# Optimization experiments

Hardware: AMD Instinct MI355X
Metric: run time of the kernel (lower is better)

The kernel has to match this reference:

```python
import jax, jax.numpy as jnp
import numpy as np


def setup_inputs() -> dict:
    key = jax.random.key(0)
    k1, k2, k3 = jax.random.split(key, 3)
    B, N = 128, 900
    x = jax.random.normal(k1, (B, N), dtype=jnp.float32)
    # true heart-rate frequencies in a realistic band (Hz)
    f_true = jax.random.uniform(k2, (B,), dtype=jnp.float32, minval=1.0, maxval=2.5)
    fs = 30.0 + jax.random.uniform(k3, (B,), dtype=jnp.float32, minval=-0.5, maxval=0.5)
    return {
        "x": x,
        "f_true": f_true,
        "fs": fs,
        "delta": 0.1,
        "sampling_f": 0.01,
        "f_min": 0.66,
        "f_max": 3.0,
    }


def _psd(freqs, x, fs, n):
    # freqs: [B, F], x: [B, N], fs: [B], n: [N]
    # Goertzel-style single-bin DFT power: (sum x*cos)^2 + (sum x*sin)^2
    ang = (2.0 * np.pi) * freqs[:, :, None] * n[None, None, :] / fs[:, None, None]  # [B,F,N]
    c = jnp.einsum('bfn,bn->bf', jnp.cos(ang), x)
    s = jnp.einsum('bfn,bn->bf', jnp.sin(ang), x)
    return c * c + s * s


def reference(x, f_true, fs, delta, sampling_f, f_min, f_max):
    B, N = x.shape
    n = jnp.arange(N, dtype=x.dtype)
    s = sampling_f

    # wanted bins: arange(f_true - delta, f_true + delta + s, s) -> static offsets around f_true
    off_w = jnp.asarray(np.arange(-delta, delta + s, s), dtype=x.dtype)  # [Fw] (~21)
    f_w = f_true[:, None] + off_w[None, :]                                # [B, Fw]

    # unwanted bins: two grids with data-dependent extents -> static max length + mask
    k_max = int(np.ceil((f_max - f_min) / s)) + 2
    k = jnp.arange(k_max, dtype=x.dtype)                                  # [K]
    f_u1 = jnp.broadcast_to(f_min + k * s, (B, k_max))                    # grid from f_min
    m1 = f_u1 < (f_true[:, None] - delta)                                 # arange end exclusive
    f_u2 = f_true[:, None] + delta + s + k[None, :] * s                   # grid from f_true+delta+s
    m2 = f_u2 < (f_max + s)

    p_w = _psd(f_w, x, fs, n)                                             # [B, Fw]
    p_u1 = _psd(f_u1, x, fs, n)                                           # [B, K]
    p_u2 = _psd(f_u2, x, fs, n)                                           # [B, K]

    term1 = p_w.mean(axis=1)
    cnt = m1.sum(axis=1) + m2.sum(axis=1)
    term2 = ((p_u1 * m1).sum(axis=1) + (p_u2 * m2).sum(axis=1)) / cnt.astype(x.dtype)
    snr = 10.0 * jnp.log10(term1 / term2)                                 # [B]
    return -snr.mean()
```

## Files before the change

### kernel.cpp

```cpp
#include <hip/hip_runtime.h>
#include <math.h>


#define WAVES 8
#define BPW   4
#define BINS_PER_BLOCK (WAVES * BPW)

template<int NG>
__global__ __launch_bounds__(64 * WAVES)
void psd_radix4(const float* __restrict__ x,
                const float* __restrict__ f_true,
                const float* __restrict__ fs,
                double* __restrict__ partW,
                double* __restrict__ partU,
                int* __restrict__ cntbuf,
                int N, int Fw, int K, int bpb, int ng_rt,
                double wstart, double wstep,
                float f_min_f, float s_f, float delta_f, float fmax_s_f)
{
    const int ng   = (NG > 0) ? NG : ng_rt;
    const int npad = ng << 8;
    extern __shared__ float xs[];
    __shared__ int    s_mc1[WAVES], s_mc2[WAVES];
    __shared__ double s_dw[WAVES], s_du[WAVES], s_inv;

    const int b    = blockIdx.x / bpb;
    const int tile = blockIdx.x - b * bpb;
    const int tid  = threadIdx.x;
    const int lane = tid & 63;
    const int w    = tid >> 6;

    for (int i = tid; i < npad; i += blockDim.x)
        xs[i] = (i < N) ? x[(size_t)b * N + i] : 0.0f;

    const float ft   = f_true[b];
    const float thr1 = __fsub_rn(ft, delta_f);

    int mc1 = 0, mc2 = 0;
    for (int i = tid; i < 2 * K; i += blockDim.x) {
        if (i < K) {
            float fu = __fadd_rn(f_min_f, __fmul_rn((float)i, s_f));
            mc1 += (fu < thr1);
        } else {
            int j = i - K;
            float fu = __fadd_rn(__fadd_rn(__fadd_rn(ft, delta_f), s_f),
                                 __fmul_rn((float)j, s_f));
            mc2 += (fu < fmax_s_f);
        }
    }
    #pragma unroll
    for (int off = 32; off; off >>= 1) {
        mc1 += __shfl_xor(mc1, off);
        mc2 += __shfl_xor(mc2, off);
    }
    if (lane == 0) { s_mc1[w] = mc1; s_mc2[w] = mc2; }
    if (tid == 0)  s_inv = 1.0 / (double)fs[b];
    __syncthreads();

    int m1 = 0, m2 = 0;
    #pragma unroll
    for (int i = 0; i < WAVES; ++i) { m1 += s_mc1[i]; m2 += s_mc2[i]; }
    const int nb = Fw + m1 + m2;
    const double inv = s_inv;

    const int u0 = (tile * WAVES + w) * BPW;

    float P[BPW], Q[BPW];
    #pragma unroll
    for (int p = 0; p < BPW; ++p) { P[p] = 0.0f; Q[p] = 0.0f; }

    if (u0 < nb) {
        float c1[BPW], s1[BPW], c2[BPW], s2[BPW], c3[BPW], s3[BPW];
        float cR[BPW], sR[BPW], Cg[BPW], Sg[BPW];
        #pragma unroll
        for (int p = 0; p < BPW; ++p) {
            const int u = u0 + p;
            float f;
            if (u < Fw)
                f = __fadd_rn(ft, (float)(wstart + (double)u * wstep));
            else if (u < Fw + m1)
                f = __fadd_rn(f_min_f, __fmul_rn((float)(u - Fw), s_f));
            else
                f = __fadd_rn(__fadd_rn(__fadd_rn(ft, delta_f), s_f),
                              __fmul_rn((float)(u - Fw - m1), s_f));
            const double r = (double)f * inv;
            double t0 = r * (double)lane; t0 -= rint(t0);
            double ts = r * 64.0;         ts -= rint(ts);
            c1[p] = __builtin_amdgcn_cosf((float)ts);
            s1[p] = __builtin_amdgcn_sinf((float)ts);
            Cg[p] = __builtin_amdgcn_cosf((float)t0);
            Sg[p] = __builtin_amdgcn_sinf((float)t0);
            c2[p] = fmaf(c1[p], c1[p], -(s1[p] * s1[p]));
            s2[p] = c1[p] * s1[p]; s2[p] += s2[p];
            c3[p] = fmaf(c2[p], c1[p], -(s2[p] * s1[p]));
            s3[p] = fmaf(s2[p], c1[p],  (c2[p] * s1[p]));
            cR[p] = fmaf(c2[p], c2[p], -(s2[p] * s2[p]));
            sR[p] = c2[p] * s2[p]; sR[p] += sR[p];
        }

        for (int g = 0; g < ng; ++g) {
            const int base = (g << 8) + lane;
            float xv0 = xs[base];
            float xv1 = xs[base + 64];
            float xv2 = xs[base + 128];
            float xv3 = xs[base + 192];
            #pragma unroll
            for (int p = 0; p < BPW; ++p) {
                float pr = fmaf(xv1, c1[p], xv0);
                pr = fmaf(xv2, c2[p], pr);
                pr = fmaf(xv3, c3[p], pr);
                float pi = xv1 * s1[p];
                pi = fmaf(xv2, s2[p], pi);
                pi = fmaf(xv3, s3[p], pi);
                P[p] = fmaf(pr, Cg[p], P[p]);
                P[p] = fmaf(-pi, Sg[p], P[p]);
                Q[p] = fmaf(pr, Sg[p], Q[p]);
                Q[p] = fmaf(pi, Cg[p], Q[p]);
                if (g != ng - 1) {
                    float cn = fmaf(Cg[p], cR[p], -(Sg[p] * sR[p]));
                    float sn = fmaf(Sg[p], cR[p],  (Cg[p] * sR[p]));
                    Cg[p] = cn; Sg[p] = sn;
                }
            }
        }
    }

    double dw = 0.0, du = 0.0;
    #pragma unroll
    for (int p = 0; p < BPW; ++p) {
        float a = P[p], q = Q[p];
        #pragma unroll
        for (int off = 32; off; off >>= 1) {
            a += __shfl_xor(a, off);
            q += __shfl_xor(q, off);
        }
        if (lane == 0) {
            const int u = u0 + p;
            if (u < nb) {
                float pw = fmaf(a, a, q * q);
                if (u < Fw) dw += (double)pw; else du += (double)pw;
            }
        }
    }
    if (lane == 0) { s_dw[w] = dw; s_du[w] = du; }
    __syncthreads();

    if (tid == 0) {
        double SW = 0.0, SU = 0.0;
        #pragma unroll
        for (int i = 0; i < WAVES; ++i) { SW += s_dw[i]; SU += s_du[i]; }
        partW[(size_t)b * bpb + tile] = SW;
        partU[(size_t)b * bpb + tile] = SU;
        if (tile == 0) cntbuf[b] = m1 + m2;
    }
}

__global__ __launch_bounds__(128)
void finish_kernel(const double* __restrict__ partW,
                   const double* __restrict__ partU,
                   const int* __restrict__ cntbuf,
                   float* __restrict__ out,
                   int Fw, int bpb, int B)
{
    const int tid  = threadIdx.x;
    const int lane = tid & 63;
    const int w    = tid >> 6;
    __shared__ double s_v[2];

    double v = 0.0;
    for (int b = tid; b < B; b += blockDim.x) {
        double SW = 0.0, SU = 0.0;
        for (int t = 0; t < bpb; ++t) {
            SW += partW[(size_t)b * bpb + t];
            SU += partU[(size_t)b * bpb + t];
        }
        v += 10.0 * log10((SW / (double)Fw) / (SU / (double)cntbuf[b]));
    }
    #pragma unroll
    for (int off = 32; off; off >>= 1) v += __shfl_xor(v, off);
    if (lane == 0) s_v[w] = v;
    __syncthreads();
    if (tid == 0) out[0] = (float)(-((s_v[0] + s_v[1]) / (double)B));
}

extern "C" void kernel_launch(void* const* d_in, const int* in_sizes, int n_in,
                              void* d_out, int out_size, void* d_ws, size_t ws_size,
                              hipStream_t stream) {
    const float* x      = (const float*)d_in[0];
    const float* f_true = (const float*)d_in[1];
    const float* fs     = (const float*)d_in[2];
    const double delta = 0.1, s = 0.01, f_min = 0.66, f_max = 3.0;

    const int B = in_sizes[1];
    const int N = in_sizes[0] / B;

    const double wstart = -delta;
    const double wstop  = delta + s;
    const double wstep  = s;
    const int Fw = (int)ceil((wstop - wstart) / wstep);
    const int K  = (int)ceil((f_max - f_min) / s) + 2;

    const int maxu  = Fw + (int)((f_max - f_min - 2.0 * delta) / s) + 8;
    const int bpb   = (maxu + BINS_PER_BLOCK - 1) / BINS_PER_BLOCK;
    const int niter = (N + 63) / 64;
    const int ng    = (niter + 3) / 4;

    const float f_min_f  = (float)f_min;
    const float s_f      = (float)s;
    const float delta_f  = (float)delta;
    const float fmax_s_f = (float)(f_max + s);

    char* base = (char*)d_ws;
    double* partW  = (double*)base;
    double* partU  = partW + (size_t)B * bpb;
    int*    cntbuf = (int*)(partU + (size_t)B * bpb);

    const size_t shmem = (size_t)ng * 256 * sizeof(float);
    dim3 grid(B * bpb), block(64 * WAVES);

    if (ng == 4)
        psd_radix4<4><<<grid, block, shmem, stream>>>(
            x, f_true, fs, partW, partU, cntbuf, N, Fw, K, bpb, ng,
            wstart, wstep, f_min_f, s_f, delta_f, fmax_s_f);
    else
        psd_radix4<0><<<grid, block, shmem, stream>>>(
            x, f_true, fs, partW, partU, cntbuf, N, Fw, K, bpb, ng,
            wstart, wstep, f_min_f, s_f, delta_f, fmax_s_f);

    finish_kernel<<<1, 128, 0, stream>>>(
        partW, partU, cntbuf, (float*)d_out, Fw, bpb, B);
}
```

Measured before the change: 18.13 us.

## Double waves per block, vectorize loads, ballot counts, and packed shuffle reductions

The block grows from 8 to 16 waves, which halves the number of blocks per batch row. The x tile is loaded into shared memory as float4, and the mask counts use ballot/popcount instead of shuffle reductions. The eight separate wave reductions of P and Q become a packed butterfly that sums several bins at once. Partials are stored as double2 and the finish kernel is templated on the tile count so its loop unrolls. The packed reduction uses fixed lane-to-bin indexing that assumes BPW==4, and the larger blocks may reduce how many blocks are resident at once.

Result: slower. 26.84 us (+48.0%).

```diff
diff --git a/kernel.cpp b/kernel.cpp
--- a/kernel.cpp
+++ b/kernel.cpp
@@ -2,17 +2,16 @@
 #include <math.h>
 
 
-#define WAVES 8
+#define WAVES 16
 #define BPW   4
 #define BINS_PER_BLOCK (WAVES * BPW)
 
 template<int NG>
-__global__ __launch_bounds__(64 * WAVES)
+__global__ __launch_bounds__(64 * WAVES, 8)
 void psd_radix4(const float* __restrict__ x,
                 const float* __restrict__ f_true,
                 const float* __restrict__ fs,
-                double* __restrict__ partW,
-                double* __restrict__ partU,
+                double2* __restrict__ part2,
                 int* __restrict__ cntbuf,
                 int N, int Fw, int K, int bpb, int ng_rt,
                 double wstart, double wstep,
@@ -21,7 +20,7 @@
     const int ng   = (NG > 0) ? NG : ng_rt;
     const int npad = ng << 8;
     extern __shared__ float xs[];
-    __shared__ int    s_mc1[WAVES], s_mc2[WAVES];
+    __shared__ int    s_c1[WAVES], s_c2[WAVES];
     __shared__ double s_dw[WAVES], s_du[WAVES], s_inv;
 
     const int b    = blockIdx.x / bpb;
@@ -30,36 +29,45 @@
     const int lane = tid & 63;
     const int w    = tid >> 6;
 
-    for (int i = tid; i < npad; i += blockDim.x)
-        xs[i] = (i < N) ? x[(size_t)b * N + i] : 0.0f;
+    {
+        const int nf4 = N >> 2;
+        float4* xs4 = reinterpret_cast<float4*>(xs);
+        const float4* xr = reinterpret_cast<const float4*>(x + (size_t)b * N);
+        for (int i = tid; i < (npad >> 2); i += blockDim.x)
+            xs4[i] = (i < nf4) ? xr[i] : make_float4(0.f, 0.f, 0.f, 0.f);
+        if (N & 3)
+            for (int i = (N & ~3) + tid; i < N; i += blockDim.x)
+                xs[i] = x[(size_t)b * N + i];
+    }
 
     const float ft   = f_true[b];
     const float thr1 = __fsub_rn(ft, delta_f);
 
-    int mc1 = 0, mc2 = 0;
-    for (int i = tid; i < 2 * K; i += blockDim.x) {
-        if (i < K) {
-            float fu = __fadd_rn(f_min_f, __fmul_rn((float)i, s_f));
-            mc1 += (fu < thr1);
-        } else {
-            int j = i - K;
-            float fu = __fadd_rn(__fadd_rn(__fadd_rn(ft, delta_f), s_f),
-                                 __fmul_rn((float)j, s_f));
-            mc2 += (fu < fmax_s_f);
-        }
-    }
-    #pragma unroll
-    for (int off = 32; off; off >>= 1) {
-        mc1 += __shfl_xor(mc1, off);
-        mc2 += __shfl_xor(mc2, off);
-    }
-    if (lane == 0) { s_mc1[w] = mc1; s_mc2[w] = mc2; }
-    if (tid == 0)  s_inv = 1.0 / (double)fs[b];
+    {
+        int c1 = 0, c2 = 0;
+        for (int i = tid; i < ((2 * K + (int)blockDim.x - 1) / (int)blockDim.x) * (int)blockDim.x;
+             i += blockDim.x) {
+            bool p1 = false, p2 = false;
+            if (i < K) {
+                float fu = __fadd_rn(f_min_f, __fmul_rn((float)i, s_f));
+                p1 = fu < thr1;
+            } else if (i < 2 * K) {
+                int j = i - K;
+                float fu = __fadd_rn(__fadd_rn(__fadd_rn(ft, delta_f), s_f),
+                                     __fmul_rn((float)j, s_f));
+                p2 = fu < fmax_s_f;
+            }
+            c1 += __popcll(__ballot(p1));
+            c2 += __popcll(__ballot(p2));
+        }
+        if (lane == 0) { s_c1[w] = c1; s_c2[w] = c2; }
+    }
+    if (tid == 0) s_inv = 1.0 / (double)fs[b];
     __syncthreads();
 
     int m1 = 0, m2 = 0;
     #pragma unroll
-    for (int i = 0; i < WAVES; ++i) { m1 += s_mc1[i]; m2 += s_mc2[i]; }
+    for (int i = 0; i < WAVES; ++i) { m1 += s_c1[i]; m2 += s_c2[i]; }
     const int nb = Fw + m1 + m2;
     const double inv = s_inv;
 
@@ -70,7 +78,7 @@
     for (int p = 0; p < BPW; ++p) { P[p] = 0.0f; Q[p] = 0.0f; }
 
     if (u0 < nb) {
-        float c1[BPW], s1[BPW], c2[BPW], s2[BPW], c3[BPW], s3[BPW];
+        float c1c[BPW], s1c[BPW], c2c[BPW], s2c[BPW], c3c[BPW], s3c[BPW];
         float cR[BPW], sR[BPW], Cg[BPW], Sg[BPW];
         #pragma unroll
         for (int p = 0; p < BPW; ++p) {
@@ -86,16 +94,16 @@
             const double r = (double)f * inv;
             double t0 = r * (double)lane; t0 -= rint(t0);
             double ts = r * 64.0;         ts -= rint(ts);
-            c1[p] = __builtin_amdgcn_cosf((float)ts);
-            s1[p] = __builtin_amdgcn_sinf((float)ts);
-            Cg[p] = __builtin_amdgcn_cosf((float)t0);
-            Sg[p] = __builtin_amdgcn_sinf((float)t0);
-            c2[p] = fmaf(c1[p], c1[p], -(s1[p] * s1[p]));
-            s2[p] = c1[p] * s1[p]; s2[p] += s2[p];
-            c3[p] = fmaf(c2[p], c1[p], -(s2[p] * s1[p]));
-            s3[p] = fmaf(s2[p], c1[p],  (c2[p] * s1[p]));
-            cR[p] = fmaf(c2[p], c2[p], -(s2[p] * s2[p]));
-            sR[p] = c2[p] * s2[p]; sR[p] += sR[p];
+            c1c[p] = __builtin_amdgcn_cosf((float)ts);
+            s1c[p] = __builtin_amdgcn_sinf((float)ts);
+            Cg[p]  = __builtin_amdgcn_cosf((float)t0);
+            Sg[p]  = __builtin_amdgcn_sinf((float)t0);
+            c2c[p] = fmaf(c1c[p], c1c[p], -(s1c[p] * s1c[p]));
+            s2c[p] = c1c[p] * s1c[p]; s2c[p] += s2c[p];
+            c3c[p] = fmaf(c2c[p], c1c[p], -(s2c[p] * s1c[p]));
+            s3c[p] = fmaf(s2c[p], c1c[p],  (c2c[p] * s1c[p]));
+            cR[p]  = fmaf(c2c[p], c2c[p], -(s2c[p] * s2c[p]));
+            sR[p]  = c2c[p] * s2c[p]; sR[p] += sR[p];
         }
 
         for (int g = 0; g < ng; ++g) {
@@ -106,12 +114,12 @@
             float xv3 = xs[base + 192];
             #pragma unroll
             for (int p = 0; p < BPW; ++p) {
-                float pr = fmaf(xv1, c1[p], xv0);
-                pr = fmaf(xv2, c2[p], pr);
-                pr = fmaf(xv3, c3[p], pr);
-                float pi = xv1 * s1[p];
-                pi = fmaf(xv2, s2[p], pi);
-                pi = fmaf(xv3, s3[p], pi);
+                float pr = fmaf(xv1, c1c[p], xv0);
+                pr = fmaf(xv2, c2c[p], pr);
+                pr = fmaf(xv3, c3c[p], pr);
+                float pi = xv1 * s1c[p];
+                pi = fmaf(xv2, s2c[p], pi);
+                pi = fmaf(xv3, s3c[p], pi);
                 P[p] = fmaf(pr, Cg[p], P[p]);
                 P[p] = fmaf(-pi, Sg[p], P[p]);
                 Q[p] = fmaf(pr, Sg[p], Q[p]);
@@ -125,62 +133,85 @@
         }
     }
 
-    double dw = 0.0, du = 0.0;
-    #pragma unroll
-    for (int p = 0; p < BPW; ++p) {
-        float a = P[p], q = Q[p];
-        #pragma unroll
-        for (int off = 32; off; off >>= 1) {
-            a += __shfl_xor(a, off);
-            q += __shfl_xor(q, off);
-        }
-        if (lane == 0) {
-            const int u = u0 + p;
-            if (u < nb) {
-                float pw = fmaf(a, a, q * q);
-                if (u < Fw) dw += (double)pw; else du += (double)pw;
-            }
-        }
-    }
-    if (lane == 0) { s_dw[w] = dw; s_du[w] = du; }
+    {
+        const bool selA = (lane & 32) != 0;
+        const bool selB = (lane & 16) != 0;
+        const bool selC = (lane & 8)  != 0;
+        float F0, F1, F2, F3, G0, G1, H;
+        { float t1 = P[0] + __shfl_xor(P[0], 32);
+          float t2 = Q[0] + __shfl_xor(Q[0], 32); F0 = selA ? t2 : t1; }
+        { float t1 = P[1] + __shfl_xor(P[1], 32);
+          float t2 = Q[1] + __shfl_xor(Q[1], 32); F1 = selA ? t2 : t1; }
+        { float t1 = P[2] + __shfl_xor(P[2], 32);
+          float t2 = Q[2] + __shfl_xor(Q[2], 32); F2 = selA ? t2 : t1; }
+        { float t1 = P[3] + __shfl_xor(P[3], 32);
+          float t2 = Q[3] + __shfl_xor(Q[3], 32); F3 = selA ? t2 : t1; }
+        { float t1 = F0 + __shfl_xor(F0, 16);
+          float t2 = F1 + __shfl_xor(F1, 16); G0 = selB ? t2 : t1; }
+        { float t1 = F2 + __shfl_xor(F2, 16);
+          float t2 = F3 + __shfl_xor(F3, 16); G1 = selB ? t2 : t1; }
+        { float t1 = G0 + __shfl_xor(G0, 8);
+          float t2 = G1 + __shfl_xor(G1, 8); H = selC ? t2 : t1; }
+        H += __shfl_xor(H, 4);
+        H += __shfl_xor(H, 2);
+        H += __shfl_xor(H, 1);
+
+        float qv = __shfl_xor(H, 32);
+        float pw = fmaf(H, H, qv * qv);
+        const int p = (((lane >> 3) & 1) << 1) | ((lane >> 4) & 1);
+        const int u = u0 + p;
+        const bool rep = ((lane & 7) == 0) && !selA;
+        float cw = (rep && u < Fw) ? pw : 0.0f;
+        float cu = (rep && u >= Fw && u < nb) ? pw : 0.0f;
+        cw += __shfl_xor(cw, 8);  cw += __shfl_xor(cw, 16);
+        cu += __shfl_xor(cu, 8);  cu += __shfl_xor(cu, 16);
+        if (lane == 0) { s_dw[w] = (double)cw; s_du[w] = (double)cu; }
+    }
     __syncthreads();
 
     if (tid == 0) {
         double SW = 0.0, SU = 0.0;
         #pragma unroll
         for (int i = 0; i < WAVES; ++i) { SW += s_dw[i]; SU += s_du[i]; }
-        partW[(size_t)b * bpb + tile] = SW;
-        partU[(size_t)b * bpb + tile] = SU;
+        double2 v; v.x = SW; v.y = SU;
+        part2[(size_t)b * bpb + tile] = v;
         if (tile == 0) cntbuf[b] = m1 + m2;
     }
 }
 
+template<int BPB>
 __global__ __launch_bounds__(128)
-void finish_kernel(const double* __restrict__ partW,
-                   const double* __restrict__ partU,
+void finish_kernel(const double2* __restrict__ part2,
                    const int* __restrict__ cntbuf,
                    float* __restrict__ out,
-                   int Fw, int bpb, int B)
+                   int Fw, int bpb_rt, int B)
 {
     const int tid  = threadIdx.x;
     const int lane = tid & 63;
-    const int w    = tid >> 6;
-    __shared__ double s_v[2];
+    __shared__ double sh[2];
 
     double v = 0.0;
     for (int b = tid; b < B; b += blockDim.x) {
         double SW = 0.0, SU = 0.0;
-        for (int t = 0; t < bpb; ++t) {
-            SW += partW[(size_t)b * bpb + t];
-            SU += partU[(size_t)b * bpb + t];
+        if (BPB > 0) {
+            #pragma unroll
+            for (int t = 0; t < BPB; ++t) {
+                double2 q = part2[b * BPB + t];
+                SW += q.x; SU += q.y;
+            }
+        } else {
+            for (int t = 0; t < bpb_rt; ++t) {
+                double2 q = part2[b * bpb_rt + t];
+                SW += q.x; SU += q.y;
+            }
         }
         v += 10.0 * log10((SW / (double)Fw) / (SU / (double)cntbuf[b]));
     }
     #pragma unroll
     for (int off = 32; off; off >>= 1) v += __shfl_xor(v, off);
-    if (lane == 0) s_v[w] = v;
+    if (lane == 0) sh[tid >> 6] = v;
     __syncthreads();
-    if (tid == 0) out[0] = (float)(-((s_v[0] + s_v[1]) / (double)B));
+    if (tid == 0) out[0] = (float)(-((sh[0] + sh[1]) / (double)B));
 }
 
 extern "C" void kernel_launch(void* const* d_in, const int* in_sizes, int n_in,
@@ -211,22 +242,25 @@
     const float fmax_s_f = (float)(f_max + s);
 
     char* base = (char*)d_ws;
-    double* partW  = (double*)base;
-    double* partU  = partW + (size_t)B * bpb;
-    int*    cntbuf = (int*)(partU + (size_t)B * bpb);
+    double2* part2  = (double2*)base;
+    int*     cntbuf = (int*)(part2 + (size_t)B * bpb);
 
     const size_t shmem = (size_t)ng * 256 * sizeof(float);
     dim3 grid(B * bpb), block(64 * WAVES);
 
     if (ng == 4)
         psd_radix4<4><<<grid, block, shmem, stream>>>(
-            x, f_true, fs, partW, partU, cntbuf, N, Fw, K, bpb, ng,
+            x, f_true, fs, part2, cntbuf, N, Fw, K, bpb, ng,
             wstart, wstep, f_min_f, s_f, delta_f, fmax_s_f);
     else
         psd_radix4<0><<<grid, block, shmem, stream>>>(
-            x, f_true, fs, partW, partU, cntbuf, N, Fw, K, bpb, ng,
+            x, f_true, fs, part2, cntbuf, N, Fw, K, bpb, ng,
             wstart, wstep, f_min_f, s_f, delta_f, fmax_s_f);
 
-    finish_kernel<<<1, 128, 0, stream>>>(
-        partW, partU, cntbuf, (float*)d_out, Fw, bpb, B);
+    if (bpb == 4)
+        finish_kernel<4><<<1, 128, 0, stream>>>(
+            part2, cntbuf, (float*)d_out, Fw, bpb, B);
+    else
+        finish_kernel<0><<<1, 128, 0, stream>>>(
+            part2, cntbuf, (float*)d_out, Fw, bpb, B);
 }
```
